# Kernel tuning notes

Hardware: AMD Instinct MI355X
Metric: run time of the kernel (lower is better)

## Reference

```python
import jax, jax.numpy as jnp
import numpy as np

# ---- fixed constants from stft2hcfp.__init__ ----
FS = 16000.0; FR = 2.0; FC = 27.5; TC = 1.0 / 4487.0; NPO = 48
N = int(FS / FR)                      # 8000 FFT length
HALF_N = int(round(N / 2))            # 4000
SQRT_N = float(np.sqrt(N))
HIGH_FREQ_IDX = int(round(1.0 / TC / FR) + 1)   # 2245
HIGH_QUEF_IDX = int(round(FS / FC)) + 1         # 583
CUT_Q = int(round(FS * TC))           # 4  (cepstrum cutoff)
TOTAL_BINS = 4 * 88                   # 352 log-freq bins
NUM_HARMONIC = 5

def _central_freqs():
    stop = 1.0 / TC
    nest = int(np.ceil(np.log2(stop / FC)) * NPO)
    cf = []
    for i in range(nest):
        c = FC * 2.0 ** (float(i) / NPO)
        if c < stop:
            cf.append(c)
        else:
            break
    return cf

CF = _central_freqs()   # 353 central frequencies
NEST = len(CF)

def _freq_matrix():
    # triangular log-frequency filterbank over linear freq axis
    f = (FS * np.linspace(0, 0.5, HALF_N, endpoint=True))[:HIGH_FREQ_IDX]
    W = np.zeros((NEST - 1, len(f)), np.float32)
    for i in range(1, NEST - 1):
        l = int(round(CF[i - 1] / FR)); r = int(round(CF[i + 1] / FR) + 1)
        if l >= r - 1:
            W[i, l] = 1.0
        else:
            for j in range(l, r):
                if CF[i - 1] < f[j] < CF[i]:
                    W[i, j] = (f[j] - CF[i - 1]) / (CF[i] - CF[i - 1])
                elif CF[i] < f[j] < CF[i + 1]:
                    W[i, j] = (CF[i + 1] - f[j]) / (CF[i + 1] - CF[i])
    return W

def _quef_matrix():
    q = np.arange(HIGH_QUEF_IDX) / FS + 1e-6
    fq = 1.0 / q
    W = np.zeros((NEST - 1, len(fq)), np.float32)
    for i in range(1, NEST - 1):
        for j in range(int(round(FS / CF[i + 1])), int(round(FS / CF[i - 1]) + 1)):
            if j >= len(fq):
                continue
            if CF[i - 1] < fq[j] < CF[i]:
                W[i, j] = (fq[j] - CF[i - 1]) / (CF[i] - CF[i - 1])
            elif CF[i] < fq[j] < CF[i + 1]:
                W[i, j] = (CF[i + 1] - fq[j]) / (CF[i + 1] - CF[i])
    return W

# harmonic shift indices: closest central freq to (k+1)*27.5 Hz, k=0..5
HIDS = [int(np.argmin(np.abs(np.asarray(CF) - (k + 1) * FC))) for k in range(NUM_HARMONIC + 1)]


def _nonlinear(x, g, cutoff):
    # relu + pow(g), then zero first/last `cutoff` rows along axis 1.
    # safe pow: grad is 0 where x<=0 (matches relu-masked torch behavior, no inf at 0)
    y = jnp.where(x > 0, jnp.where(x > 0, x, 1.0) ** g, 0.0)
    y = y.at[:, :cutoff].set(0.0).at[:, -cutoff:].set(0.0)
    return y


def setup_inputs() -> dict:
    key = jax.random.key(0)
    dx = jax.random.uniform(key, (8, 512, N), dtype=jnp.float32)  # [B, T, 8000] spectrogram
    return {
        "dx": dx,
        "W_freq": jnp.asarray(_freq_matrix()),   # [352, 2245]
        "W_quef": jnp.asarray(_quef_matrix()),   # [352, 583]
    }


def reference(dx, W_freq, W_quef):
    tfr0 = jnp.swapaxes(dx, 1, 2)                       # [B, F=8000, T]
    # CFP layer 1: real part of FFT over freq axis -> cepstrum, nonlinear g=0.6
    ceps = jnp.fft.fft(tfr0, axis=1).real / SQRT_N      # [B, 8000, T]
    ceps = _nonlinear(ceps, 0.6, CUT_Q)
    # log-frequency mappings (banded triangular filterbanks)
    tfr0h = tfr0[:, :HIGH_FREQ_IDX]                      # [B, 2245, T]
    cepsh = ceps[:, :HIGH_QUEF_IDX]                      # [B, 583, T]
    tfrL0 = jnp.einsum('kf,bft->bkt', W_freq, tfr0h)     # [B, 352, T]
    tfrLQ = jnp.einsum('kq,bqt->bkt', W_quef, cepsh)     # [B, 352, T]
    # harmonic stacking: shift down (spectral) / shift up (cepstral)
    har_s = [jnp.pad(tfrL0[:, h:TOTAL_BINS], ((0, 0), (0, h), (0, 0))) for h in HIDS]
    har_c = [jnp.pad(tfrLQ[:, :TOTAL_BINS - h], ((0, 0), (h, 0), (0, 0))) for h in HIDS]
    piece = jnp.concatenate([jnp.stack(har_s, axis=1), jnp.stack(har_c, axis=1)], axis=1)
    return jnp.swapaxes(piece, 2, 3)                     # [B, 12, T, 352]
```

## Files before the change

kernel.cpp:

```cpp
#include <hip/hip_runtime.h>
#include <hip/hip_bf16.h>
#include <limits.h>

typedef __attribute__((ext_vector_type(8))) short short8;
typedef __attribute__((ext_vector_type(4))) float f32x4;
typedef __attribute__((ext_vector_type(16))) float f32x16;

#define NN 8000
#define NCOL 4096
#define KBINS 352
#define QPAD 640
#define QH 320
#define BN 256
#define KC 8
#define NTILE 64
#define KSTEP 8
#define CUTQ 4
#define T_ 512
#define WFB 64
#define WQB 20
#define NFB 2048
#define NCB 640

#define GLL16(g, l) __builtin_amdgcn_global_load_lds( \
    (const __attribute__((address_space(1))) unsigned int*)(g), \
    (__attribute__((address_space(3))) unsigned int*)(l), 16, 0, 0)

static __device__ __forceinline__ ushort bfc(float f){
  __hip_bfloat16 h = __float2bfloat16(f);
  return *reinterpret_cast<ushort*>(&h);
}
static __device__ __forceinline__ float b2f(ushort u){
  unsigned v = ((unsigned)u) << 16; float f; __builtin_memcpy(&f, &v, 4); return f;
}

__global__ __launch_bounds__(256) void prep_k(const float* __restrict__ dx,
        ushort* __restrict__ xf, ushort* __restrict__ cosg,
        const float* __restrict__ Wf, const float* __restrict__ Wq,
        int HFI, int HQI, int* __restrict__ fLo, int* __restrict__ qLo,
        float* __restrict__ WfT, float* __restrict__ WqT){
  int blk = blockIdx.x, t = threadIdx.x;
  if (blk < NFB){
    int flat = blk*256 + t;
    int row = flat >> 7, batch = flat & 127;
    int n0 = batch*32;
    const float* rp = dx + (size_t)row*NN;
    f32x4 F[8], M[8];
    #pragma unroll
    for (int i=0;i<8;i++) F[i] = *(const f32x4*)(rp + n0 + 4*i);
    #pragma unroll
    for (int i=0;i<8;i++) M[i] = *(const f32x4*)(rp + 7968 - n0 + 4*i);
    float s = n0 ? rp[NN - n0] : 0.f;
    int kt = n0 >> 6;
    int s8b = (batch & 1) * 4;
    ushort* xrow = xf + ((size_t)kt*NCOL + row)*64;
    int swz = (row & 7) << 3;
    #pragma unroll
    for (int j=0;j<4;j++){
      short8 o;
      #pragma unroll
      for (int e=0;e<8;e++){
        int n = n0 + 8*j + e;
        float fwd = F[2*j + (e>>2)][e & 3];
        int mi = 32 - 8*j - e;
        float mir = (mi == 32) ? s : M[mi >> 2][mi & 3];
        float v = (n < 4000) ? fwd + mir : ((n == 4000) ? fwd : 0.f);
        o[e] = (short)bfc(v);
      }
      *(short8*)(&xrow[(((s8b + j) << 3) ^ swz)]) = o;
    }
  } else if (blk < NFB + NCB){
    int q = blk - NFB;
    int qz = (q < HQI) ? 1 : 0;
    #pragma unroll
    for (int h=0; h<2; ++h){
      int n0 = t*16 + h*8;
      short8 o;
      #pragma unroll
      for (int e=0;e<8;e++){
        float v = 0.f;
        if (qz){
          int m = (q*(n0+e)) % NN;
          v = cosf((float)m * 7.8539816339744831e-4f);
        }
        o[e] = (short)bfc(v);
      }
      int kt = n0 >> 6, s8 = (n0 >> 3) & 7;
      *(short8*)(&cosg[(size_t)kt*(QPAD*64) + (size_t)q*64 + ((s8 ^ (q & 7)) << 3)]) = o;
    }
  } else {
    __shared__ int slo, shi;
    int u = blk - NFB - NCB;
    int r = u >> 1;
    bool isF = (u & 1) == 0;
    const float* W = isF ? Wf : Wq;
    int width = isF ? HFI : HQI;
    int bw    = isF ? WFB : WQB;
    float* WT = isF ? WfT : WqT;
    int* Lo   = isF ? fLo : qLo;
    if (t==0){ slo = INT_MAX; shi = -1; }
    __syncthreads();
    int mylo = INT_MAX, myhi = -1;
    for (int c = t; c < width; c += 256){
      if (W[(size_t)r*width + c] != 0.f){ if (c < mylo) mylo = c; if (c > myhi) myhi = c; }
    }
    atomicMin(&slo, mylo); atomicMax(&shi, myhi);
    __syncthreads();
    int l = (shi < 0) ? 0 : slo, h = (shi < 0) ? 0 : shi + 1;
    if (t==0) Lo[r] = l;
    for (int j = t; j < bw; j += 256){
      float v = 0.f;
      if (l + j < h) v = W[(size_t)r*width + l + j];
      WT[(size_t)j*KBINS + r] = v;
    }
  }
}

__global__ __launch_bounds__(512, 2) void gemm_k(const ushort* __restrict__ xf,
                                                 const ushort* __restrict__ cosg,
                                                 ushort* __restrict__ part){
  __shared__ ushort As[2][QH*64];
  __shared__ ushort Bs[2][BN*64];
  int tid = threadIdx.x;
  int nb = blockIdx.x, qh = blockIdx.y, kc = blockIdx.z;
  int lane = tid & 63, widx = tid >> 6;
  int wm = widx & 1, wn = widx >> 1;
  int l31 = lane & 31, lh = lane >> 5;
  int kt0 = kc*KSTEP, ktE = kt0 + KSTEP;

  const ushort* ag0 = cosg + (size_t)qh*(QH*64) + tid*8;
  const ushort* bg0 = xf + (size_t)nb*(BN*64) + tid*8;

  #define STAGE(kt_, buf_) { \
    const ushort* ag_ = ag0 + (size_t)(kt_)*(QPAD*64); \
    _Pragma("unroll") \
    for (int i_=0;i_<5;i_++) GLL16(ag_ + i_*4096, &As[buf_][tid*8 + i_*4096]); \
    const ushort* bg_ = bg0 + (size_t)(kt_)*(NCOL*64); \
    _Pragma("unroll") \
    for (int i_=0;i_<4;i_++) GLL16(bg_ + i_*4096, &Bs[buf_][tid*8 + i_*4096]); }

  f32x16 acc[5][2];
  #pragma unroll
  for (int a=0;a<5;a++){ acc[a][0] = (f32x16)0.f; acc[a][1] = (f32x16)0.f; }

  STAGE(kt0, 0);

  int cur = 0;
  for (int kt = kt0; kt < ktE; ++kt){
    if (kt + 1 < ktE){
      STAGE(kt+1, cur^1);
      asm volatile("s_waitcnt vmcnt(9)" ::: "memory");
    } else {
      asm volatile("s_waitcnt vmcnt(0)" ::: "memory");
    }
    __builtin_amdgcn_s_barrier();
    __builtin_amdgcn_sched_barrier(0);
    const ushort* Ac = &As[cur][0];
    const ushort* Bc = &Bs[cur][0];
    #pragma unroll
    for (int p=0;p<4;p++){
      short8 dfr[2];
      #pragma unroll
      for (int c=0;c<2;c++){
        int row = wn*64 + c*32 + l31;
        dfr[c] = *(const short8*)(Bc + row*64 + ((((p<<1)|lh) ^ (row & 7)) << 3));
      }
      short8 cfr[5];
      #pragma unroll
      for (int a=0;a<5;a++){
        int row = wm*160 + a*32 + l31;
        cfr[a] = *(const short8*)(Ac + row*64 + ((((p<<1)|lh) ^ (row & 7)) << 3));
      }
      __builtin_amdgcn_s_setprio(1);
      #pragma unroll
      for (int a=0;a<5;a++){
        acc[a][0] = __builtin_amdgcn_mfma_f32_32x32x16_bf16(dfr[0], cfr[a], acc[a][0], 0,0,0);
        acc[a][1] = __builtin_amdgcn_mfma_f32_32x32x16_bf16(dfr[1], cfr[a], acc[a][1], 0,0,0);
      }
      __builtin_amdgcn_s_setprio(0);
      __builtin_amdgcn_sched_barrier(0);
      __builtin_amdgcn_s_barrier();
      __builtin_amdgcn_sched_barrier(0);
    }
    cur ^= 1;
  }

  ushort* pb = part + (size_t)kc*NCOL*QPAD;
  #pragma unroll
  for (int a=0;a<5;a++){
    int q = qh*QH + wm*160 + a*32 + l31;
    #pragma unroll
    for (int c=0;c<2;c++){
      int colb = nb*BN + wn*64 + c*32 + 4*lh;
      #pragma unroll
      for (int r=0;r<16;r++){
        int col = colb + (r&3) + 8*(r>>2);
        pb[(size_t)col*QPAD + q] = bfc(acc[a][c][r]);
      }
    }
  }
}

__global__ __launch_bounds__(384) void fuse_k(const float* __restrict__ dx,
        const ushort* __restrict__ part,
        const float* __restrict__ WfT, const float* __restrict__ WqT,
        const int* __restrict__ fLo, const int* __restrict__ qLo,
        float* __restrict__ out, int HFI, int HQI){
  __shared__ float xr[2368];
  __shared__ float yq[QPAD];
  __shared__ float tl0[KBINS];
  __shared__ float tlq[KBINS];
  int col = blockIdx.x;
  int b = col >> 9, t = col & 511;
  int tid = threadIdx.x;
  const float invs = 0.011180339887498949f;

  for (int f = tid; f < 2368; f += 384) xr[f] = (f < HFI) ? dx[(size_t)col*NN + f] : 0.f;
  const ushort* pc = part + (size_t)col*QPAD;
  for (int q = tid; q < QPAD; q += 384){
    float y = 0.f;
    if (q < HQI){
      float s = 0.f;
      #pragma unroll
      for (int kc=0; kc<KC; kc++) s += b2f(pc[(size_t)kc*NCOL*QPAD + q]);
      s *= invs;
      if (q >= CUTQ && s > 0.f) y = powf(s, 0.6f);
    }
    yq[q] = y;
  }
  __syncthreads();

  if (tid < KBINS){
    int k = tid;
    int lo = fLo[k];
    float aF = 0.f;
    #pragma unroll
    for (int j=0;j<WFB;j++) aF += WfT[j*KBINS + k] * xr[lo + j];
    int ql = qLo[k];
    float aQ = 0.f;
    #pragma unroll
    for (int j=0;j<WQB;j++) aQ += WqT[j*KBINS + k] * yq[ql + j];
    tl0[k] = aF; tlq[k] = aQ;
  }
  __syncthreads();

  const int hids[6] = {0,48,76,96,111,124};
  for (int u = tid; u < 12*KBINS; u += 384){
    int j = u / KBINS;
    int k = u - j*KBINS;
    int h = hids[(j < 6) ? j : j - 6];
    float v;
    if (j < 6) v = (k + h < KBINS) ? tl0[k + h] : 0.f;
    else       v = (k >= h)        ? tlq[k - h] : 0.f;
    out[(((size_t)b*12 + j)*T_ + t)*KBINS + k] = v;
  }
}

extern "C" void kernel_launch(void* const* d_in, const int* in_sizes, int n_in,
                              void* d_out, int out_size, void* d_ws, size_t ws_size,
                              hipStream_t stream){
  const float* dx = (const float*)d_in[0];
  const float* Wf = (const float*)d_in[1];
  const float* Wq = (const float*)d_in[2];
  int HFI = in_sizes[1] / KBINS;
  int HQI = in_sizes[2] / KBINS;
  float* out = (float*)d_out;
  char* ws = (char*)d_ws;

  ushort* cosg = (ushort*)ws;
  size_t off = (size_t)NTILE*QPAD*64*2;
  ushort* xf = (ushort*)(ws + off); off += (size_t)NTILE*NCOL*64*2;
  ushort* part = (ushort*)(ws + off); off += (size_t)KC*NCOL*QPAD*2;
  int* fLo = (int*)(ws+off); off += KBINS*4;
  int* qLo = (int*)(ws+off); off += KBINS*4;
  float* WfT = (float*)(ws+off); off += (size_t)WFB*KBINS*4;
  float* WqT = (float*)(ws+off); off += (size_t)WQB*KBINS*4;
  (void)n_in; (void)out_size; (void)ws_size;

  prep_k<<<NFB + NCB + 2*KBINS, 256, 0, stream>>>(dx, xf, cosg, Wf, Wq,
                                                  HFI, HQI, fLo, qLo, WfT, WqT);
  gemm_k<<<dim3(NCOL/BN, QPAD/QH, KC), 512, 0, stream>>>(xf, cosg, part);
  fuse_k<<<NCOL, 384, 0, stream>>>(dx, part, WfT, WqT, fLo, qLo, out, HFI, HQI);
}
```

Baseline: 136.0 us.

## Store folded input row-major and stage B tiles through registers with swizzled LDS writes

The prep kernel now uses one block per input row and builds the mirrored sum with wave shuffles. It writes the folded bf16 data in a plain row-major [row, 4096] layout instead of the pre-tiled swizzled layout, giving coalesced prep writes. The GEMM loads B tiles into registers with ordinary global loads and then writes them into LDS with the XOR swizzle. The A tile still uses direct global-to-LDS loads. This also changes the barrier schedule so the next tile's LDS write happens after compute, at the cost of extra register pressure and a B write phase exposed at the end of each k-step.

```diff
diff --git a/kernel.cpp b/kernel.cpp
--- a/kernel.cpp
+++ b/kernel.cpp
@@ -4,6 +4,7 @@
 
 typedef __attribute__((ext_vector_type(8))) short short8;
 typedef __attribute__((ext_vector_type(4))) float f32x4;
+typedef __attribute__((ext_vector_type(4))) int i32x4;
 typedef __attribute__((ext_vector_type(16))) float f32x16;
 
 #define NN 8000
@@ -15,11 +16,12 @@
 #define KC 8
 #define NTILE 64
 #define KSTEP 8
+#define XROW 4096
 #define CUTQ 4
 #define T_ 512
 #define WFB 64
 #define WQB 20
-#define NFB 2048
+#define NFB 4096
 #define NCB 640
 
 #define GLL16(g, l) __builtin_amdgcn_global_load_lds( \
@@ -41,33 +43,47 @@
         float* __restrict__ WfT, float* __restrict__ WqT){
   int blk = blockIdx.x, t = threadIdx.x;
   if (blk < NFB){
-    int flat = blk*256 + t;
-    int row = flat >> 7, batch = flat & 127;
-    int n0 = batch*32;
+    int row = blk;
+    int w = t >> 6, l = t & 63;
     const float* rp = dx + (size_t)row*NN;
-    f32x4 F[8], M[8];
-    #pragma unroll
-    for (int i=0;i<8;i++) F[i] = *(const f32x4*)(rp + n0 + 4*i);
-    #pragma unroll
-    for (int i=0;i<8;i++) M[i] = *(const f32x4*)(rp + 7968 - n0 + 4*i);
-    float s = n0 ? rp[NN - n0] : 0.f;
-    int kt = n0 >> 6;
-    int s8b = (batch & 1) * 4;
-    ushort* xrow = xf + ((size_t)kt*NCOL + row)*64;
-    int swz = (row & 7) << 3;
-    #pragma unroll
-    for (int j=0;j<4;j++){
+    ushort* xrow = xf + (size_t)row*XROW;
+    f32x4 F0[2], F1[2], M0[2], M1[2];
+    int n0g[2], N0g[2];
+    #pragma unroll
+    for (int g=0; g<2; ++g){
+      int N0 = (2*w + g)*512;
+      int n0 = N0 + 8*l;
+      N0g[g] = N0; n0g[g] = n0;
+      F0[g] = *(const f32x4*)(rp + n0);
+      F1[g] = *(const f32x4*)(rp + n0 + 4);
+      int mb = 8000 - N0 - 511 + 8*l;
+      bool sh = (N0 == 0 && l == 63);
+      M0[g] = *(const f32x4*)(rp + mb);
+      M1[g] = *(const f32x4*)(rp + mb + (sh ? 3 : 4));
+    }
+    #pragma unroll
+    for (int g=0; g<2; ++g){
+      float a[8];
+      #pragma unroll
+      for (int i=0;i<4;i++) a[i]   = __shfl(M0[g][i], 63 - l, 64);
+      #pragma unroll
+      for (int i=0;i<4;i++) a[4+i] = __shfl(M1[g][i], 63 - l, 64);
+      float fw[8] = {F0[g][0],F0[g][1],F0[g][2],F0[g][3],F1[g][0],F1[g][1],F1[g][2],F1[g][3]};
+      bool comp = (N0g[g] == 0 && l == 0);
       short8 o;
       #pragma unroll
       for (int e=0;e<8;e++){
-        int n = n0 + 8*j + e;
-        float fwd = F[2*j + (e>>2)][e & 3];
-        int mi = 32 - 8*j - e;
-        float mir = (mi == 32) ? s : M[mi >> 2][mi & 3];
-        float v = (n < 4000) ? fwd + mir : ((n == 4000) ? fwd : 0.f);
+        int n = n0g[g] + e;
+        int mi = 7 - e;
+        if (comp && e >= 1 && e <= 4) mi = 8 - e;
+        float v;
+        if (n == 0)          v = fw[0];
+        else if (n < 4000)   v = fw[e] + a[mi];
+        else if (n == 4000)  v = fw[e];
+        else                 v = 0.f;
         o[e] = (short)bfc(v);
       }
-      *(short8*)(&xrow[(((s8b + j) << 3) ^ swz)]) = o;
+      *(short8*)(xrow + n0g[g]) = o;
     }
   } else if (blk < NFB + NCB){
     int q = blk - NFB;
@@ -129,31 +145,41 @@
   int kt0 = kc*KSTEP, ktE = kt0 + KSTEP;
 
   const ushort* ag0 = cosg + (size_t)qh*(QH*64) + tid*8;
-  const ushort* bg0 = xf + (size_t)nb*(BN*64) + tid*8;
-
-  #define STAGE(kt_, buf_) { \
+  int brow0 = tid >> 3, bs = tid & 7;
+  const ushort* bg0 = xf + ((size_t)(nb*BN + brow0))*XROW + bs*8;
+  int bw0 = brow0*64 + ((bs ^ (brow0 & 7)) << 3);
+
+  i32x4 Breg[4];
+  #define AGLL(kt_, buf_) { \
     const ushort* ag_ = ag0 + (size_t)(kt_)*(QPAD*64); \
     _Pragma("unroll") \
-    for (int i_=0;i_<5;i_++) GLL16(ag_ + i_*4096, &As[buf_][tid*8 + i_*4096]); \
-    const ushort* bg_ = bg0 + (size_t)(kt_)*(NCOL*64); \
+    for (int i_=0;i_<5;i_++) GLL16(ag_ + i_*4096, &As[buf_][tid*8 + i_*4096]); }
+  #define BLOAD(kt_) { \
     _Pragma("unroll") \
-    for (int i_=0;i_<4;i_++) GLL16(bg_ + i_*4096, &Bs[buf_][tid*8 + i_*4096]); }
+    for (int i_=0;i_<4;i_++) Breg[i_] = *(const i32x4*)(bg0 + (size_t)i_*64*XROW + (kt_)*64); }
+  #define BWRITE(buf_) { \
+    _Pragma("unroll") \
+    for (int i_=0;i_<4;i_++) *(i32x4*)(&Bs[buf_][bw0 + i_*4096]) = Breg[i_]; }
 
   f32x16 acc[5][2];
   #pragma unroll
   for (int a=0;a<5;a++){ acc[a][0] = (f32x16)0.f; acc[a][1] = (f32x16)0.f; }
 
-  STAGE(kt0, 0);
+  BLOAD(kt0);
+  AGLL(kt0, 0);
+  asm volatile("s_waitcnt vmcnt(5)" ::: "memory");
+  BWRITE(0);
+  asm volatile("s_waitcnt vmcnt(0) lgkmcnt(0)" ::: "memory");
+  __builtin_amdgcn_s_barrier();
+  __builtin_amdgcn_sched_barrier(0);
 
   int cur = 0;
   for (int kt = kt0; kt < ktE; ++kt){
-    if (kt + 1 < ktE){
-      STAGE(kt+1, cur^1);
-      asm volatile("s_waitcnt vmcnt(9)" ::: "memory");
-    } else {
-      asm volatile("s_waitcnt vmcnt(0)" ::: "memory");
-    }
-    __builtin_amdgcn_s_barrier();
+    bool stg = (kt + 1 < ktE);
+    if (stg){
+      BLOAD(kt+1);
+      AGLL(kt+1, cur^1);
+    }
     __builtin_amdgcn_sched_barrier(0);
     const ushort* Ac = &As[cur][0];
     const ushort* Bc = &Bs[cur][0];
@@ -178,7 +204,17 @@
         acc[a][1] = __builtin_amdgcn_mfma_f32_32x32x16_bf16(dfr[1], cfr[a], acc[a][1], 0,0,0);
       }
       __builtin_amdgcn_s_setprio(0);
+      if (p < 3){
+        __builtin_amdgcn_sched_barrier(0);
+        __builtin_amdgcn_s_barrier();
+        __builtin_amdgcn_sched_barrier(0);
+      }
+    }
+    if (stg){
       __builtin_amdgcn_sched_barrier(0);
+      asm volatile("s_waitcnt vmcnt(5)" ::: "memory");
+      BWRITE(cur^1);
+      asm volatile("s_waitcnt vmcnt(0) lgkmcnt(0)" ::: "memory");
       __builtin_amdgcn_s_barrier();
       __builtin_amdgcn_sched_barrier(0);
     }
@@ -269,7 +305,7 @@
 
   ushort* cosg = (ushort*)ws;
   size_t off = (size_t)NTILE*QPAD*64*2;
-  ushort* xf = (ushort*)(ws + off); off += (size_t)NTILE*NCOL*64*2;
+  ushort* xf = (ushort*)(ws + off); off += (size_t)NCOL*XROW*2;
   ushort* part = (ushort*)(ws + off); off += (size_t)KC*NCOL*QPAD*2;
   int* fLo = (int*)(ws+off); off += KBINS*4;
   int* qLo = (int*)(ws+off); off += KBINS*4;
```

Result: faster. 125.2 us (median of 2 runs) (-7.9%).

## Fuse even-symmetric input folding and bf16 conversion into GEMM B-tile staging

Applied to the files above, without the earlier changes.

The pass that folded dx into a symmetric bf16 staging buffer (xf) is removed from prep_k. gemm_k now loads the fp32 forward and mirrored samples straight from dx into registers, folds and converts them, and writes the swizzled tile into LDS for the next k-step. This drops the xf write and re-read round trip through global memory. In exchange the B path is register-staged rather than async LDS loads, adds a full vmcnt(0) wait and an extra barrier per k-step, and reads dx with scattered mirrored loads, all of which may hurt overlap.

```diff
diff --git a/kernel.cpp b/kernel.cpp
--- a/kernel.cpp
+++ b/kernel.cpp
@@ -19,7 +19,6 @@
 #define T_ 512
 #define WFB 64
 #define WQB 20
-#define NFB 2048
 #define NCB 640
 
 #define GLL16(g, l) __builtin_amdgcn_global_load_lds( \
@@ -34,43 +33,13 @@
   unsigned v = ((unsigned)u) << 16; float f; __builtin_memcpy(&f, &v, 4); return f;
 }
 
-__global__ __launch_bounds__(256) void prep_k(const float* __restrict__ dx,
-        ushort* __restrict__ xf, ushort* __restrict__ cosg,
+__global__ __launch_bounds__(256) void prep_k(ushort* __restrict__ cosg,
         const float* __restrict__ Wf, const float* __restrict__ Wq,
         int HFI, int HQI, int* __restrict__ fLo, int* __restrict__ qLo,
         float* __restrict__ WfT, float* __restrict__ WqT){
   int blk = blockIdx.x, t = threadIdx.x;
-  if (blk < NFB){
-    int flat = blk*256 + t;
-    int row = flat >> 7, batch = flat & 127;
-    int n0 = batch*32;
-    const float* rp = dx + (size_t)row*NN;
-    f32x4 F[8], M[8];
-    #pragma unroll
-    for (int i=0;i<8;i++) F[i] = *(const f32x4*)(rp + n0 + 4*i);
-    #pragma unroll
-    for (int i=0;i<8;i++) M[i] = *(const f32x4*)(rp + 7968 - n0 + 4*i);
-    float s = n0 ? rp[NN - n0] : 0.f;
-    int kt = n0 >> 6;
-    int s8b = (batch & 1) * 4;
-    ushort* xrow = xf + ((size_t)kt*NCOL + row)*64;
-    int swz = (row & 7) << 3;
-    #pragma unroll
-    for (int j=0;j<4;j++){
-      short8 o;
-      #pragma unroll
-      for (int e=0;e<8;e++){
-        int n = n0 + 8*j + e;
-        float fwd = F[2*j + (e>>2)][e & 3];
-        int mi = 32 - 8*j - e;
-        float mir = (mi == 32) ? s : M[mi >> 2][mi & 3];
-        float v = (n < 4000) ? fwd + mir : ((n == 4000) ? fwd : 0.f);
-        o[e] = (short)bfc(v);
-      }
-      *(short8*)(&xrow[(((s8b + j) << 3) ^ swz)]) = o;
-    }
-  } else if (blk < NFB + NCB){
-    int q = blk - NFB;
+  if (blk < NCB){
+    int q = blk;
     int qz = (q < HQI) ? 1 : 0;
     #pragma unroll
     for (int h=0; h<2; ++h){
@@ -90,7 +59,7 @@
     }
   } else {
     __shared__ int slo, shi;
-    int u = blk - NFB - NCB;
+    int u = blk - NCB;
     int r = u >> 1;
     bool isF = (u & 1) == 0;
     const float* W = isF ? Wf : Wq;
@@ -116,7 +85,7 @@
   }
 }
 
-__global__ __launch_bounds__(512, 2) void gemm_k(const ushort* __restrict__ xf,
+__global__ __launch_bounds__(512, 2) void gemm_k(const float* __restrict__ dx,
                                                  const ushort* __restrict__ cosg,
                                                  ushort* __restrict__ part){
   __shared__ ushort As[2][QH*64];
@@ -129,31 +98,64 @@
   int kt0 = kc*KSTEP, ktE = kt0 + KSTEP;
 
   const ushort* ag0 = cosg + (size_t)qh*(QH*64) + tid*8;
-  const ushort* bg0 = xf + (size_t)nb*(BN*64) + tid*8;
-
-  #define STAGE(kt_, buf_) { \
+  int brow0 = tid >> 3, bs = tid & 7;
+  const float* bp0 = dx + (size_t)(nb*BN + brow0)*NN;
+  int bw0 = brow0*64 + ((bs ^ (brow0 & 7)) << 3);
+
+  f32x4 BF0[4], BF1[4], BMA[4], BMB[4];
+  float BMS[4];
+
+  #define AGLL(kt_, buf_) { \
     const ushort* ag_ = ag0 + (size_t)(kt_)*(QPAD*64); \
     _Pragma("unroll") \
-    for (int i_=0;i_<5;i_++) GLL16(ag_ + i_*4096, &As[buf_][tid*8 + i_*4096]); \
-    const ushort* bg_ = bg0 + (size_t)(kt_)*(NCOL*64); \
+    for (int i_=0;i_<5;i_++) GLL16(ag_ + i_*4096, &As[buf_][tid*8 + i_*4096]); }
+  #define BLOAD(kt_) { int n0_ = (kt_)*64 + bs*8; \
     _Pragma("unroll") \
-    for (int i_=0;i_<4;i_++) GLL16(bg_ + i_*4096, &Bs[buf_][tid*8 + i_*4096]); }
+    for (int i_=0;i_<4;i_++){ \
+      const float* rp_ = bp0 + (size_t)i_*64*NN; \
+      BF0[i_] = *(const f32x4*)(rp_ + n0_); \
+      BF1[i_] = *(const f32x4*)(rp_ + n0_ + 4); \
+      BMA[i_] = *(const f32x4*)(rp_ + 7996 - n0_); \
+      BMB[i_] = *(const f32x4*)(rp_ + 7992 - n0_); \
+      BMS[i_] = rp_[n0_ ? NN - n0_ : 0]; } }
+  #define BWRITE(kt_, buf_) { int n0_ = (kt_)*64 + bs*8; \
+    _Pragma("unroll") \
+    for (int i_=0;i_<4;i_++){ \
+      float pr_[8] = {BF0[i_][0],BF0[i_][1],BF0[i_][2],BF0[i_][3], \
+                      BF1[i_][0],BF1[i_][1],BF1[i_][2],BF1[i_][3]}; \
+      float mi_[8] = {n0_ ? BMS[i_] : 0.f, BMA[i_][3],BMA[i_][2],BMA[i_][1],BMA[i_][0], \
+                      BMB[i_][3],BMB[i_][2],BMB[i_][1]}; \
+      short8 o_; \
+      _Pragma("unroll") \
+      for (int e_=0;e_<8;e_++){ \
+        int n_ = n0_ + e_; \
+        float v_; \
+        if (n_ == 0)          v_ = pr_[0]; \
+        else if (n_ < 4000)   v_ = pr_[e_] + mi_[e_]; \
+        else if (n_ == 4000)  v_ = pr_[e_]; \
+        else                  v_ = 0.f; \
+        o_[e_] = (short)bfc(v_); } \
+      *(short8*)(&Bs[buf_][bw0 + i_*4096]) = o_; } }
 
   f32x16 acc[5][2];
   #pragma unroll
   for (int a=0;a<5;a++){ acc[a][0] = (f32x16)0.f; acc[a][1] = (f32x16)0.f; }
 
-  STAGE(kt0, 0);
+  BLOAD(kt0);
+  AGLL(kt0, 0);
+  asm volatile("s_waitcnt vmcnt(0)" ::: "memory");
+  BWRITE(kt0, 0);
+  asm volatile("s_waitcnt lgkmcnt(0)" ::: "memory");
+  __builtin_amdgcn_s_barrier();
+  __builtin_amdgcn_sched_barrier(0);
 
   int cur = 0;
   for (int kt = kt0; kt < ktE; ++kt){
-    if (kt + 1 < ktE){
-      STAGE(kt+1, cur^1);
-      asm volatile("s_waitcnt vmcnt(9)" ::: "memory");
-    } else {
-      asm volatile("s_waitcnt vmcnt(0)" ::: "memory");
-    }
-    __builtin_amdgcn_s_barrier();
+    bool stg = (kt + 1 < ktE);
+    if (stg){
+      BLOAD(kt+1);
+      AGLL(kt+1, cur^1);
+    }
     __builtin_amdgcn_sched_barrier(0);
     const ushort* Ac = &As[cur][0];
     const ushort* Bc = &Bs[cur][0];
@@ -178,7 +180,17 @@
         acc[a][1] = __builtin_amdgcn_mfma_f32_32x32x16_bf16(dfr[1], cfr[a], acc[a][1], 0,0,0);
       }
       __builtin_amdgcn_s_setprio(0);
+      if (p < 3){
+        __builtin_amdgcn_sched_barrier(0);
+        __builtin_amdgcn_s_barrier();
+        __builtin_amdgcn_sched_barrier(0);
+      }
+    }
+    if (stg){
       __builtin_amdgcn_sched_barrier(0);
+      asm volatile("s_waitcnt vmcnt(0)" ::: "memory");
+      BWRITE(kt+1, cur^1);
+      asm volatile("s_waitcnt lgkmcnt(0)" ::: "memory");
       __builtin_amdgcn_s_barrier();
       __builtin_amdgcn_sched_barrier(0);
     }
@@ -269,7 +281,6 @@
 
   ushort* cosg = (ushort*)ws;
   size_t off = (size_t)NTILE*QPAD*64*2;
-  ushort* xf = (ushort*)(ws + off); off += (size_t)NTILE*NCOL*64*2;
   ushort* part = (ushort*)(ws + off); off += (size_t)KC*NCOL*QPAD*2;
   int* fLo = (int*)(ws+off); off += KBINS*4;
   int* qLo = (int*)(ws+off); off += KBINS*4;
@@ -277,8 +288,7 @@
   float* WqT = (float*)(ws+off); off += (size_t)WQB*KBINS*4;
   (void)n_in; (void)out_size; (void)ws_size;
 
-  prep_k<<<NFB + NCB + 2*KBINS, 256, 0, stream>>>(dx, xf, cosg, Wf, Wq,
-                                                  HFI, HQI, fLo, qLo, WfT, WqT);
-  gemm_k<<<dim3(NCOL/BN, QPAD/QH, KC), 512, 0, stream>>>(xf, cosg, part);
+  prep_k<<<NCB + 2*KBINS, 256, 0, stream>>>(cosg, Wf, Wq, HFI, HQI, fLo, qLo, WfT, WqT);
+  gemm_k<<<dim3(NCOL/BN, QPAD/QH, KC), 512, 0, stream>>>(dx, cosg, part);
   fuse_k<<<NCOL, 384, 0, stream>>>(dx, part, WfT, WqT, fLo, qLo, out, HFI, HQI);
 }
```

After: 167.8 us. 23.4% more time.
